# Kernel tuning notes

Hardware: AMD Instinct MI355X
Metric: run time of the kernel (lower is better)

## Reference

```python
import jax, jax.numpy as jnp
import numpy as np

B, C, T = 8, 1024, 1500          # batch, WavLM feature dim, frames
K = 8192                         # linguistic centroid bank size
D, H = 256, 512                  # refiner embed dim, MLP hidden dim
NQ, BINS = 4, 1024               # RVQ stages, codebook bins per stage
LRELU_SLOPE = 0.01               # torch LeakyReLU default
EPS = 1e-8


def setup_inputs():
    key = jax.random.key(0)
    ks = jax.random.split(key, 24)
    w = lambda k, s: jax.random.normal(k, s, dtype=jnp.float32) * 0.02
    inp = {
        'feature': jax.random.normal(ks[0], (B, C, T), dtype=jnp.float32),
        'centroid': jax.random.normal(ks[1], (K, C), dtype=jnp.float32),
        # SpeakerRefiner encoder: 1024->512->512->256 (LeakyReLU between)
        'enc_w0': w(ks[2], (C, H)), 'enc_b0': w(ks[3], (H,)),
        'enc_w1': w(ks[4], (H, H)), 'enc_b1': w(ks[5], (H,)),
        'enc_w2': w(ks[6], (H, D)), 'enc_b2': w(ks[7], (D,)),
        # SpeakerRefiner decoder: 256->512->512->1024 (LeakyReLU between)
        'dec_w0': w(ks[8], (D, H)), 'dec_b0': w(ks[9], (H,)),
        'dec_w1': w(ks[10], (H, H)), 'dec_b1': w(ks[11], (H,)),
        'dec_w2': w(ks[12], (H, C)), 'dec_b2': w(ks[13], (C,)),
        # SpeakerNormalizer: 1024->512->512->256, ReLU after EVERY layer
        'nrm_w0': w(ks[14], (C, H)), 'nrm_b0': w(ks[15], (H,)),
        'nrm_w1': w(ks[16], (H, H)), 'nrm_b1': w(ks[17], (H,)),
        'nrm_w2': w(ks[18], (H, D)), 'nrm_b2': w(ks[19], (D,)),
        # RVQ codebooks, one per stage
        'codebooks': jax.random.normal(ks[20], (NQ, BINS, D), dtype=jnp.float32),
    }
    return inp


def _nn_gather(x_flat, table):
    """argmin of squared distances (x^2 - 2 x.C^T + C^2) + row gather."""
    dist = ((x_flat ** 2).sum(1, keepdims=True)
            - 2.0 * x_flat @ table.T
            + (table ** 2).sum(1)[None, :])
    idx = jnp.argmin(dist, axis=1)
    return table[idx]


def reference(feature, centroid,
              enc_w0, enc_b0, enc_w1, enc_b1, enc_w2, enc_b2,
              dec_w0, dec_b0, dec_w1, dec_b1, dec_w2, dec_b2,
              nrm_w0, nrm_b0, nrm_w1, nrm_b1, nrm_w2, nrm_b2,
              codebooks):
    lrelu = lambda v: jax.nn.leaky_relu(v, LRELU_SLOPE)

    def enc(z):  # (B,T,C) -> (B,T,D)
        h0 = lrelu(z @ enc_w0 + enc_b0)
        h1 = lrelu(h0 @ enc_w1 + enc_b1)
        return h1 @ enc_w2 + enc_b2

    def dec(z):  # (B,T,D) -> (B,T,C)
        h0 = lrelu(z @ dec_w0 + dec_b0)
        h1 = lrelu(h0 @ dec_w1 + dec_b1)
        return h1 @ dec_w2 + dec_b2

    def nrm(z):  # (B,T,C) -> (B,T,D), ReLU after each Linear
        h0 = jax.nn.relu(z @ nrm_w0 + nrm_b0)
        h1 = jax.nn.relu(h0 @ nrm_w1 + nrm_b1)
        return jax.nn.relu(h1 @ nrm_w2 + nrm_b2)

    # ---- linguistic VQ: cdist + argmin + gather over centroid bank ----
    x_flat = feature.transpose(0, 2, 1).reshape(-1, C)        # (B*T, C)
    lin_dec_bt = _nn_gather(x_flat, centroid).reshape(B, T, C)  # (B,T,C)
    lin_dec = lin_dec_bt.transpose(0, 2, 1)                    # (B,C,T)

    # ---- speaker residual path ----
    spk_raw = feature - lin_dec                                # (B,C,T)
    spk_enc = enc(spk_raw.transpose(0, 2, 1))                  # (B,T,D)
    norm_vec = nrm(lin_dec_bt)                                 # (B,T,D)  (iteration > norm_start_step branch)
    spk_enc_norm = spk_enc / (norm_vec + EPS)

    # ---- residual vector quantizer (n_q stages, straight-through) ----
    residual, q_sum = spk_enc_norm, jnp.zeros_like(spk_enc_norm)
    for i in range(NQ):
        q = _nn_gather(residual.reshape(-1, D), codebooks[i]).reshape(B, T, D)
        q_sum = q_sum + q
        residual = residual - q
    quantized = spk_enc_norm + jax.lax.stop_gradient(q_sum - spk_enc_norm)

    # ---- denorm + decode + combine ----
    spk_enc_denorm = quantized * norm_vec
    spk_dec = dec(spk_enc_denorm).transpose(0, 2, 1)           # (B,C,T)
    dec_feature = lin_dec + spk_dec                            # quantize == [1,1]
    return dec_feature
```

## Files before the change

### kernel.cpp

```cpp
#include <hip/hip_runtime.h>

namespace {

constexpr int kB = 8;
constexpr int kC = 1024;
constexpr int kT = 1500;
constexpr int kK = 8192;
constexpr int kD = 256;
constexpr int kH = 512;
constexpr int kNQ = 4;
constexpr int kBins = 1024;
constexpr int kN = kB * kT;
constexpr float kEps = 1e-8f;
constexpr float kSlope = 0.01f;
constexpr float kMargin = 8.0f;
constexpr unsigned kCap = 4194304;

using u64 = unsigned long long;
typedef __attribute__((ext_vector_type(8))) short bf16x8;
typedef __attribute__((ext_vector_type(4))) float f32x4;

__device__ __forceinline__ unsigned ordered_bits(float f) {
  unsigned b = __float_as_uint(f);
  return (b & 0x80000000u) ? ~b : (b | 0x80000000u);
}
__device__ __forceinline__ float unordered_bits(unsigned b) {
  return __uint_as_float((b & 0x80000000u) ? (b ^ 0x80000000u) : ~b);
}
__device__ __forceinline__ unsigned short f2bf(float f) {
  unsigned u = __float_as_uint(f);
  return (unsigned short)((u + 0x7fffu + ((u >> 16) & 1u)) >> 16);
}
__device__ __forceinline__ void gl_lds16(const void* g, void* l) {
  __builtin_amdgcn_global_load_lds(
      (const __attribute__((address_space(1))) void*)g,
      (__attribute__((address_space(3))) void*)l, 16, 0, 0);
}

__global__ __launch_bounds__(256) void transpose_in(const float* __restrict__ f,
                                                    float* __restrict__ X) {
  __shared__ float tile[32][33];
  const int t0 = blockIdx.x * 32, c0 = blockIdx.y * 32, b = blockIdx.z;
  const int tx = threadIdx.x, ty = threadIdx.y;
#pragma unroll
  for (int i = 0; i < 4; ++i) {
    const int cl = ty + i * 8;
    if (t0 + tx < kT)
      tile[cl][tx] = f[(size_t)b * kC * kT + (size_t)(c0 + cl) * kT + (t0 + tx)];
  }
  __syncthreads();
#pragma unroll
  for (int i = 0; i < 4; ++i) {
    const int tl = ty + i * 8;
    if (t0 + tl < kT)
      X[(size_t)(b * kT + t0 + tl) * kC + (c0 + tx)] = tile[tx][tl];
  }
}

__global__ __launch_bounds__(256) void to_bf16(const float* __restrict__ in,
                                               unsigned short* __restrict__ out,
                                               int n4) {
  const int i = blockIdx.x * 256 + threadIdx.x;
  if (i >= n4) return;
  const float4 v = reinterpret_cast<const float4*>(in)[i];
  ushort4 o;
  o.x = f2bf(v.x); o.y = f2bf(v.y); o.z = f2bf(v.z); o.w = f2bf(v.w);
  reinterpret_cast<ushort4*>(out)[i] = o;
}

__global__ __launch_bounds__(256) void row_sqsum(const float* __restrict__ A,
                                                 float* __restrict__ S, int Kd) {
  const int r = blockIdx.x;
  const float4* a4 = reinterpret_cast<const float4*>(A + (size_t)r * Kd);
  float s = 0.f;
  for (int i = threadIdx.x; i < (Kd >> 2); i += 256) {
    const float4 v = a4[i];
    s = fmaf(v.x, v.x, s); s = fmaf(v.y, v.y, s);
    s = fmaf(v.z, v.z, s); s = fmaf(v.w, v.w, s);
  }
#pragma unroll
  for (int off = 32; off > 0; off >>= 1) s += __shfl_down(s, off, 64);
  __shared__ float ws[4];
  const int lane = threadIdx.x & 63, w = threadIdx.x >> 6;
  if (lane == 0) ws[w] = s;
  __syncthreads();
  if (threadIdx.x == 0) S[r] = (ws[0] + ws[1]) + (ws[2] + ws[3]);
}

__global__ __launch_bounds__(256) void lin_vq_mfma(
    const unsigned short* __restrict__ Ah, const unsigned short* __restrict__ Bh,
    const float* __restrict__ S, const float* __restrict__ cc,
    unsigned* __restrict__ rowmin, unsigned* __restrict__ cands,
    unsigned* __restrict__ counter, int M) {
  __shared__ __attribute__((aligned(16))) unsigned short lsa[128 * 32];
  __shared__ __attribute__((aligned(16))) unsigned short lsb[128 * 32];
  const int t = threadIdx.x;
  const int l = t & 63, w = t >> 6;
  const int wr = w >> 1, wc = w & 1;
  const int m0 = blockIdx.x * 128, n0 = blockIdx.y * 128;
  const int rl = l & 15, lh = l >> 4;
  const int srow = l >> 2, sp = l & 3;
  f32x4 acc[4][4] = {};
  for (int k0 = 0; k0 < kC; k0 += 32) {
#pragma unroll
    for (int i = 0; i < 2; ++i) {
      const int rb = (w * 2 + i) * 16;
      const int r = rb + srow;
      const int s = (sp - ((r >> 1) & 3)) & 3;
      gl_lds16(Ah + ((size_t)(m0 + r) * kC + k0 + s * 8), &lsa[rb * 32]);
      gl_lds16(Bh + ((size_t)(n0 + r) * kC + k0 + s * 8), &lsb[rb * 32]);
    }
    __syncthreads();
    bf16x8 a[4], b[4];
#pragma unroll
    for (int m = 0; m < 4; ++m) {
      const int r = wr * 64 + m * 16 + rl;
      const int pp = (lh + ((r >> 1) & 3)) & 3;
      a[m] = *reinterpret_cast<const bf16x8*>(&lsa[r * 32 + pp * 8]);
    }
#pragma unroll
    for (int n = 0; n < 4; ++n) {
      const int r = wc * 64 + n * 16 + rl;
      const int pp = (lh + ((r >> 1) & 3)) & 3;
      b[n] = *reinterpret_cast<const bf16x8*>(&lsb[r * 32 + pp * 8]);
    }
#pragma unroll
    for (int m = 0; m < 4; ++m)
#pragma unroll
      for (int n = 0; n < 4; ++n)
        acc[m][n] = __builtin_amdgcn_mfma_f32_16x16x32_bf16(a[m], b[n], acc[m][n], 0, 0, 0);
    __syncthreads();
  }
  float ccv[4];
#pragma unroll
  for (int n = 0; n < 4; ++n) ccv[n] = cc[n0 + wc * 64 + n * 16 + rl];
#pragma unroll
  for (int m = 0; m < 4; ++m) {
#pragma unroll
    for (int j = 0; j < 4; ++j) {
      const int gr = m0 + wr * 64 + m * 16 + lh * 4 + j;
      const bool valid = gr < M;
      const float Sv = valid ? S[gr] : 0.f;
      float mn = 3.4e38f;
#pragma unroll
      for (int n = 0; n < 4; ++n) {
        const float d = fmaf(-2.f, acc[m][n][j], Sv) + ccv[n];
        acc[m][n][j] = d;
        mn = fminf(mn, d);
      }
#pragma unroll
      for (int mask = 1; mask < 16; mask <<= 1)
        mn = fminf(mn, __shfl_xor(mn, mask, 64));
      if (valid && rl == 0) atomicMin(&rowmin[gr], ordered_bits(mn));
    }
  }
  __threadfence();
#pragma unroll
  for (int m = 0; m < 4; ++m) {
#pragma unroll
    for (int j = 0; j < 4; ++j) {
      const int gr = m0 + wr * 64 + m * 16 + lh * 4 + j;
      if (gr >= M) continue;
      const float thr = unordered_bits(rowmin[gr]) + kMargin;
#pragma unroll
      for (int n = 0; n < 4; ++n) {
        if (acc[m][n][j] <= thr) {
          const unsigned gc = (unsigned)(n0 + wc * 64 + n * 16 + rl);
          const unsigned slot = atomicAdd(counter, 1u);
          if (slot < kCap) cands[slot] = (unsigned)gr * 8192u + gc;
        }
      }
    }
  }
}

__global__ __launch_bounds__(256) void rescore(
    const float* __restrict__ X, const float* __restrict__ Cn,
    const float* __restrict__ S, const float* __restrict__ cc,
    const unsigned* __restrict__ cands, const unsigned* __restrict__ counter,
    u64* __restrict__ keys) {
  const unsigned nc = min(*counter, kCap);
  const int l = threadIdx.x & 63;
  const unsigned wglob = (blockIdx.x * 256 + threadIdx.x) >> 6;
  const unsigned nw = (gridDim.x * 256) >> 6;
  for (unsigned i = wglob; i < nc; i += nw) {
    const unsigned pc = cands[i];
    const int r = pc >> 13, c = pc & 8191;
    const float4* xr = reinterpret_cast<const float4*>(X + (size_t)r * kC);
    const float4* cr = reinterpret_cast<const float4*>(Cn + (size_t)c * kC);
    float acc = 0.f;
#pragma unroll
    for (int q = 0; q < 4; ++q) {
      const float4 a = xr[l * 4 + q], b = cr[l * 4 + q];
      acc = fmaf(a.x, b.x, acc); acc = fmaf(a.y, b.y, acc);
      acc = fmaf(a.z, b.z, acc); acc = fmaf(a.w, b.w, acc);
    }
#pragma unroll
    for (int off = 32; off > 0; off >>= 1) acc += __shfl_down(acc, off, 64);
    if (l == 0) {
      const float d = (S[r] - 2.0f * acc) + cc[c];
      atomicMin(&keys[r], ((u64)ordered_bits(d) << 32) | (unsigned)c);
    }
  }
}

__global__ __launch_bounds__(256) void vq_argmin(
    const float* __restrict__ A, const float* __restrict__ table,
    const float* __restrict__ cc, const float* __restrict__ S,
    u64* __restrict__ keys, int M, int Kd) {
  __shared__ float As[16][128];
  __shared__ float Ts[16][128];
  __shared__ u64 red[128][16];
  const int m0 = blockIdx.x * 128, n0 = blockIdx.y * 128;
  const int t = threadIdx.x;
  const int tx = t & 15, ty = t >> 4;
  const int lrow = t >> 1, lk8 = (t & 1) * 8;
  float acc[8][8] = {};
  for (int k0 = 0; k0 < Kd; k0 += 16) {
    const int gm = m0 + lrow;
    float4 a0 = make_float4(0.f, 0.f, 0.f, 0.f), a1 = a0;
    if (gm < M) {
      const float* ap = &A[(size_t)gm * Kd + (k0 + lk8)];
      a0 = *reinterpret_cast<const float4*>(ap);
      a1 = *reinterpret_cast<const float4*>(ap + 4);
    }
    const float* tp = &table[(size_t)(n0 + lrow) * Kd + (k0 + lk8)];
    const float4 b0 = *reinterpret_cast<const float4*>(tp);
    const float4 b1 = *reinterpret_cast<const float4*>(tp + 4);
    As[lk8 + 0][lrow] = a0.x; As[lk8 + 1][lrow] = a0.y;
    As[lk8 + 2][lrow] = a0.z; As[lk8 + 3][lrow] = a0.w;
    As[lk8 + 4][lrow] = a1.x; As[lk8 + 5][lrow] = a1.y;
    As[lk8 + 6][lrow] = a1.z; As[lk8 + 7][lrow] = a1.w;
    Ts[lk8 + 0][lrow] = b0.x; Ts[lk8 + 1][lrow] = b0.y;
    Ts[lk8 + 2][lrow] = b0.z; Ts[lk8 + 3][lrow] = b0.w;
    Ts[lk8 + 4][lrow] = b1.x; Ts[lk8 + 5][lrow] = b1.y;
    Ts[lk8 + 6][lrow] = b1.z; Ts[lk8 + 7][lrow] = b1.w;
    __syncthreads();
#pragma unroll
    for (int kk = 0; kk < 16; ++kk) {
      float ar[8], br[8];
      *reinterpret_cast<float4*>(&ar[0]) = *reinterpret_cast<const float4*>(&As[kk][ty * 8]);
      *reinterpret_cast<float4*>(&ar[4]) = *reinterpret_cast<const float4*>(&As[kk][ty * 8 + 4]);
      *reinterpret_cast<float4*>(&br[0]) = *reinterpret_cast<const float4*>(&Ts[kk][tx * 8]);
      *reinterpret_cast<float4*>(&br[4]) = *reinterpret_cast<const float4*>(&Ts[kk][tx * 8 + 4]);
#pragma unroll
      for (int i = 0; i < 8; ++i)
#pragma unroll
        for (int j = 0; j < 8; ++j) acc[i][j] = fmaf(ar[i], br[j], acc[i][j]);
    }
    __syncthreads();
  }
  float ccv[8];
  *reinterpret_cast<float4*>(&ccv[0]) = *reinterpret_cast<const float4*>(&cc[n0 + tx * 8]);
  *reinterpret_cast<float4*>(&ccv[4]) = *reinterpret_cast<const float4*>(&cc[n0 + tx * 8 + 4]);
#pragma unroll
  for (int i = 0; i < 8; ++i) {
    const int gm = m0 + ty * 8 + i;
    const float Srow = (gm < M) ? S[gm] : 0.f;
    u64 best = ~0ull;
#pragma unroll
    for (int j = 0; j < 8; ++j) {
      const int gn = n0 + tx * 8 + j;
      const float d = (Srow - 2.0f * acc[i][j]) + ccv[j];
      const u64 key = ((u64)ordered_bits(d) << 32) | (unsigned)gn;
      best = (key < best) ? key : best;
    }
    red[ty * 8 + i][tx] = best;
  }
  __syncthreads();
  if (t < 128) {
    u64 b = red[t][0];
#pragma unroll
    for (int j = 1; j < 16; ++j) { const u64 v = red[t][j]; b = (v < b) ? v : b; }
    const int gm = m0 + t;
    if (gm < M) atomicMin(&keys[gm], b);
  }
}

__global__ __launch_bounds__(256) void gather_residual(
    const float* __restrict__ centroid, const u64* __restrict__ keys,
    float* __restrict__ X, float* __restrict__ lin_dec) {
  const int i4 = blockIdx.x * 256 + threadIdx.x;
  const int n = i4 >> 8;
  const int c4 = (i4 & 255) << 2;
  const unsigned idx = (unsigned)(keys[n] & 0xffffffffu);
  const float4 cv = *reinterpret_cast<const float4*>(&centroid[(size_t)idx * kC + c4]);
  float4 xv = *reinterpret_cast<const float4*>(&X[(size_t)n * kC + c4]);
  xv.x -= cv.x; xv.y -= cv.y; xv.z -= cv.z; xv.w -= cv.w;
  *reinterpret_cast<float4*>(&lin_dec[(size_t)n * kC + c4]) = cv;
  *reinterpret_cast<float4*>(&X[(size_t)n * kC + c4]) = xv;
}

template <int ACT>
__global__ __launch_bounds__(256) void gemm_bias_act(
    const float* __restrict__ A, const float* __restrict__ W,
    const float* __restrict__ bias, float* __restrict__ out,
    int M, int Nc, int Kd) {
  __shared__ float As[16][64];
  __shared__ float Ws[16][64];
  const int m0 = blockIdx.x * 64, n0 = blockIdx.y * 64;
  const int t = threadIdx.x;
  const int tx = t & 15, ty = t >> 4;
  const int arow = t >> 2, ak4 = (t & 3) << 2;
  const int wk = t >> 4, wn4 = (t & 15) << 2;
  float acc[4][4] = {};
  for (int k0 = 0; k0 < Kd; k0 += 16) {
    float4 av = make_float4(0.f, 0.f, 0.f, 0.f);
    const int gm = m0 + arow;
    if (gm < M) av = *reinterpret_cast<const float4*>(&A[(size_t)gm * Kd + (k0 + ak4)]);
    As[ak4 + 0][arow] = av.x; As[ak4 + 1][arow] = av.y;
    As[ak4 + 2][arow] = av.z; As[ak4 + 3][arow] = av.w;
    *reinterpret_cast<float4*>(&Ws[wk][wn4]) =
        *reinterpret_cast<const float4*>(&W[(size_t)(k0 + wk) * Nc + (n0 + wn4)]);
    __syncthreads();
#pragma unroll
    for (int kk = 0; kk < 16; ++kk) {
      float ar[4], br[4];
      *reinterpret_cast<float4*>(ar) = *reinterpret_cast<const float4*>(&As[kk][ty << 2]);
      *reinterpret_cast<float4*>(br) = *reinterpret_cast<const float4*>(&Ws[kk][tx << 2]);
#pragma unroll
      for (int i = 0; i < 4; ++i)
#pragma unroll
        for (int j = 0; j < 4; ++j) acc[i][j] = fmaf(ar[i], br[j], acc[i][j]);
    }
    __syncthreads();
  }
  float bv[4];
  *reinterpret_cast<float4*>(bv) = *reinterpret_cast<const float4*>(&bias[n0 + (tx << 2)]);
#pragma unroll
  for (int i = 0; i < 4; ++i) {
    const int gm = m0 + (ty << 2) + i;
    if (gm >= M) continue;
    float o[4];
#pragma unroll
    for (int j = 0; j < 4; ++j) {
      float v = acc[i][j] + bv[j];
      if (ACT == 1) v = (v >= 0.f) ? v : kSlope * v;
      if (ACT == 2) v = fmaxf(v, 0.f);
      o[j] = v;
    }
    *reinterpret_cast<float4*>(&out[(size_t)gm * Nc + n0 + (tx << 2)]) =
        *reinterpret_cast<const float4*>(o);
  }
}

__global__ __launch_bounds__(256) void norm_div_init(
    const float* __restrict__ e, const float* __restrict__ nv,
    float* __restrict__ resid, float* __restrict__ qsum) {
  const int i = blockIdx.x * 256 + threadIdx.x;
  const float4 ev = reinterpret_cast<const float4*>(e)[i];
  const float4 vv = reinterpret_cast<const float4*>(nv)[i];
  float4 r;
  r.x = ev.x / (vv.x + kEps); r.y = ev.y / (vv.y + kEps);
  r.z = ev.z / (vv.z + kEps); r.w = ev.w / (vv.w + kEps);
  reinterpret_cast<float4*>(resid)[i] = r;
  reinterpret_cast<float4*>(qsum)[i] = make_float4(0.f, 0.f, 0.f, 0.f);
}

__global__ __launch_bounds__(256) void rvq_update(
    const float* __restrict__ cb, const u64* __restrict__ keys,
    float* __restrict__ resid, float* __restrict__ qsum) {
  const int i4 = blockIdx.x * 256 + threadIdx.x;
  const int n = i4 >> 6;
  const int d4 = (i4 & 63) << 2;
  const unsigned idx = (unsigned)(keys[n] & 0xffffffffu);
  const float4 q = *reinterpret_cast<const float4*>(&cb[(size_t)idx * kD + d4]);
  float4 r = reinterpret_cast<float4*>(resid)[i4];
  float4 s = reinterpret_cast<float4*>(qsum)[i4];
  r.x -= q.x; r.y -= q.y; r.z -= q.z; r.w -= q.w;
  s.x += q.x; s.y += q.y; s.z += q.z; s.w += q.w;
  reinterpret_cast<float4*>(resid)[i4] = r;
  reinterpret_cast<float4*>(qsum)[i4] = s;
}

__global__ __launch_bounds__(256) void denorm(
    const float* __restrict__ qsum, const float* __restrict__ nv,
    float* __restrict__ o) {
  const int i = blockIdx.x * 256 + threadIdx.x;
  const float4 q = reinterpret_cast<const float4*>(qsum)[i];
  const float4 v = reinterpret_cast<const float4*>(nv)[i];
  float4 r;
  r.x = q.x * v.x; r.y = q.y * v.y; r.z = q.z * v.z; r.w = q.w * v.w;
  reinterpret_cast<float4*>(o)[i] = r;
}

__global__ __launch_bounds__(256) void final_out(const float* __restrict__ lin_dec,
                                                 const float* __restrict__ dec_out,
                                                 float* __restrict__ out) {
  __shared__ float tile[32][33];
  const int t0 = blockIdx.x * 32, c0 = blockIdx.y * 32, b = blockIdx.z;
  const int tx = threadIdx.x, ty = threadIdx.y;
#pragma unroll
  for (int i = 0; i < 4; ++i) {
    const int tl = ty + i * 8;
    if (t0 + tl < kT) {
      const size_t idx = (size_t)(b * kT + t0 + tl) * kC + (c0 + tx);
      tile[tl][tx] = lin_dec[idx] + dec_out[idx];
    }
  }
  __syncthreads();
#pragma unroll
  for (int i = 0; i < 4; ++i) {
    const int cl = ty + i * 8;
    if (t0 + tx < kT)
      out[(size_t)b * kC * kT + (size_t)(c0 + cl) * kT + (t0 + tx)] = tile[tx][cl];
  }
}

}

extern "C" void kernel_launch(void* const* d_in, const int* in_sizes, int n_in,
                              void* d_out, int out_size, void* d_ws, size_t ws_size,
                              hipStream_t stream) {
  (void)in_sizes; (void)n_in; (void)out_size; (void)ws_size;
  const float* feature  = (const float*)d_in[0];
  const float* centroid = (const float*)d_in[1];
  const float* enc_w0 = (const float*)d_in[2];  const float* enc_b0 = (const float*)d_in[3];
  const float* enc_w1 = (const float*)d_in[4];  const float* enc_b1 = (const float*)d_in[5];
  const float* enc_w2 = (const float*)d_in[6];  const float* enc_b2 = (const float*)d_in[7];
  const float* dec_w0 = (const float*)d_in[8];  const float* dec_b0 = (const float*)d_in[9];
  const float* dec_w1 = (const float*)d_in[10]; const float* dec_b1 = (const float*)d_in[11];
  const float* dec_w2 = (const float*)d_in[12]; const float* dec_b2 = (const float*)d_in[13];
  const float* nrm_w0 = (const float*)d_in[14]; const float* nrm_b0 = (const float*)d_in[15];
  const float* nrm_w1 = (const float*)d_in[16]; const float* nrm_b1 = (const float*)d_in[17];
  const float* nrm_w2 = (const float*)d_in[18]; const float* nrm_b2 = (const float*)d_in[19];
  const float* codebooks = (const float*)d_in[20];
  float* out = (float*)d_out;

  float* X       = (float*)d_ws;
  float* lin_dec = X       + (size_t)kN * kC;
  float* h0      = lin_dec + (size_t)kN * kC;
  float* h1      = h0      + (size_t)kN * kH;
  float* e_out   = h1      + (size_t)kN * kH;
  float* nvec    = e_out   + (size_t)kN * kD;
  float* resid   = nvec    + (size_t)kN * kD;
  float* qsum    = resid   + (size_t)kN * kD;
  float* Srow    = qsum    + (size_t)kN * kD;
  float* ccbuf   = Srow    + kN;
  u64*   keys    = (u64*)(ccbuf + kK);

  unsigned short* xh = (unsigned short*)h0;
  unsigned short* ch = (unsigned short*)h1;
  unsigned* cands    = (unsigned*)lin_dec;
  unsigned* rowmin   = (unsigned*)(h1 + 4500000);
  unsigned* counter  = rowmin + kN;

  const dim3 tb32(32, 8);
  const dim3 tgT((kT + 31) / 32, kC / 32, kB);

  transpose_in<<<tgT, tb32, 0, stream>>>(feature, X);

  row_sqsum<<<kN, 256, 0, stream>>>(X, Srow, kC);
  row_sqsum<<<kK, 256, 0, stream>>>(centroid, ccbuf, kC);
  to_bf16<<<(kN * kC / 4 + 255) / 256, 256, 0, stream>>>(X, xh, kN * kC / 4);
  to_bf16<<<(kK * kC / 4 + 255) / 256, 256, 0, stream>>>(centroid, ch, kK * kC / 4);
  hipMemsetAsync(rowmin, 0xFF, (size_t)kN * sizeof(unsigned), stream);
  hipMemsetAsync(counter, 0x00, sizeof(unsigned), stream);
  hipMemsetAsync(keys, 0xFF, (size_t)kN * sizeof(u64), stream);
  lin_vq_mfma<<<dim3((kN + 127) / 128, kK / 128), 256, 0, stream>>>(
      xh, ch, Srow, ccbuf, rowmin, cands, counter, kN);
  rescore<<<512, 256, 0, stream>>>(X, centroid, Srow, ccbuf, cands, counter, keys);
  gather_residual<<<kN * kC / 4 / 256, 256, 0, stream>>>(centroid, keys, X, lin_dec);

  const dim3 gH((kN + 63) / 64, kH / 64);
  const dim3 gD((kN + 63) / 64, kD / 64);
  const dim3 gC((kN + 63) / 64, kC / 64);

  gemm_bias_act<1><<<gH, 256, 0, stream>>>(X,  enc_w0, enc_b0, h0,    kN, kH, kC);
  gemm_bias_act<1><<<gH, 256, 0, stream>>>(h0, enc_w1, enc_b1, h1,    kN, kH, kH);
  gemm_bias_act<0><<<gD, 256, 0, stream>>>(h1, enc_w2, enc_b2, e_out, kN, kD, kH);

  gemm_bias_act<2><<<gH, 256, 0, stream>>>(lin_dec, nrm_w0, nrm_b0, h0,   kN, kH, kC);
  gemm_bias_act<2><<<gH, 256, 0, stream>>>(h0,      nrm_w1, nrm_b1, h1,   kN, kH, kH);
  gemm_bias_act<2><<<gD, 256, 0, stream>>>(h1,      nrm_w2, nrm_b2, nvec, kN, kD, kH);

  norm_div_init<<<kN * kD / 4 / 256, 256, 0, stream>>>(e_out, nvec, resid, qsum);

  for (int q = 0; q < kNQ; ++q) {
    const float* cb = codebooks + (size_t)q * kBins * kD;
    row_sqsum<<<kN, 256, 0, stream>>>(resid, Srow, kD);
    row_sqsum<<<kBins, 256, 0, stream>>>(cb, ccbuf, kD);
    hipMemsetAsync(keys, 0xFF, (size_t)kN * sizeof(u64), stream);
    vq_argmin<<<dim3((kN + 127) / 128, kBins / 128), 256, 0, stream>>>(
        resid, cb, ccbuf, Srow, keys, kN, kD);
    rvq_update<<<kN * kD / 4 / 256, 256, 0, stream>>>(cb, keys, resid, qsum);
  }

  denorm<<<kN * kD / 4 / 256, 256, 0, stream>>>(qsum, nvec, e_out);

  gemm_bias_act<1><<<gH, 256, 0, stream>>>(e_out, dec_w0, dec_b0, h0, kN, kH, kD);
  gemm_bias_act<1><<<gH, 256, 0, stream>>>(h0,    dec_w1, dec_b1, h1, kN, kH, kH);
  gemm_bias_act<0><<<gC, 256, 0, stream>>>(h1,    dec_w2, dec_b2, X,  kN, kC, kH);

  final_out<<<tgT, tb32, 0, stream>>>(lin_dec, X, out);
}
```

Measured before the change: 2.794 ms.

## Move decoder MLP to bf16 MFMA GEMMs and double-buffer the centroid search GEMM

The three decoder GEMMs move from the fp32 gemm_bias_act kernel to a new bf16 MFMA kernel. It uses double-buffered LDS staging and writes bf16 intermediate activations. The decoder weights are transposed to bf16 on device, and the denorm step now writes bf16 directly. The lin_vq_mfma kernel gets double-buffered async global-to-LDS loads and a block-index swizzle that groups blocks for cache locality. The change trades decoder precision (bf16 inputs and hidden states) for matrix-core throughput, and adds a few small transpose launches.

```diff
diff --git a/kernel.cpp b/kernel.cpp
--- a/kernel.cpp
+++ b/kernel.cpp
@@ -37,6 +37,19 @@
       (__attribute__((address_space(3))) void*)l, 16, 0, 0);
 }
 
+__device__ __forceinline__ void stage_tile(const unsigned short* __restrict__ g,
+                                           int rowlen, int r0, int k0,
+                                           unsigned short* lds,
+                                           int w, int srow, int sp) {
+#pragma unroll
+  for (int i = 0; i < 2; ++i) {
+    const int rb = (w * 2 + i) * 16;
+    const int r = rb + srow;
+    const int s = (sp - ((r >> 1) & 3)) & 3;
+    gl_lds16(g + ((size_t)(r0 + r) * rowlen + k0 + s * 8), lds + rb * 32);
+  }
+}
+
 __global__ __launch_bounds__(256) void transpose_in(const float* __restrict__ f,
                                                     float* __restrict__ X) {
   __shared__ float tile[32][33];
@@ -68,6 +81,20 @@
   reinterpret_cast<ushort4*>(out)[i] = o;
 }
 
+__global__ __launch_bounds__(256) void transpose_w_bf16(
+    const float* __restrict__ W, unsigned short* __restrict__ WT, int K, int N) {
+  __shared__ float tile[32][33];
+  const int k0 = blockIdx.x * 32, n0 = blockIdx.y * 32;
+  const int tx = threadIdx.x, ty = threadIdx.y;
+#pragma unroll
+  for (int i = 0; i < 4; ++i)
+    tile[ty + i * 8][tx] = W[(size_t)(k0 + ty + i * 8) * N + (n0 + tx)];
+  __syncthreads();
+#pragma unroll
+  for (int i = 0; i < 4; ++i)
+    WT[(size_t)(n0 + ty + i * 8) * K + (k0 + tx)] = f2bf(tile[tx][ty + i * 8]);
+}
+
 __global__ __launch_bounds__(256) void row_sqsum(const float* __restrict__ A,
                                                  float* __restrict__ S, int Kd) {
   const int r = blockIdx.x;
@@ -92,37 +119,41 @@
     const float* __restrict__ S, const float* __restrict__ cc,
     unsigned* __restrict__ rowmin, unsigned* __restrict__ cands,
     unsigned* __restrict__ counter, int M) {
-  __shared__ __attribute__((aligned(16))) unsigned short lsa[128 * 32];
-  __shared__ __attribute__((aligned(16))) unsigned short lsb[128 * 32];
+  __shared__ __attribute__((aligned(16))) unsigned short lsa[2][128 * 32];
+  __shared__ __attribute__((aligned(16))) unsigned short lsb[2][128 * 32];
   const int t = threadIdx.x;
   const int l = t & 63, w = t >> 6;
   const int wr = w >> 1, wc = w & 1;
-  const int m0 = blockIdx.x * 128, n0 = blockIdx.y * 128;
   const int rl = l & 15, lh = l >> 4;
   const int srow = l >> 2, sp = l & 3;
+  const unsigned nbx = gridDim.x;
+  const unsigned flat = blockIdx.y * nbx + blockIdx.x;
+  const unsigned q8 = (nbx * gridDim.y) >> 3;
+  const unsigned swz = (flat & 7u) * q8 + (flat >> 3);
+  const int m0 = (int)(swz % nbx) * 128, n0 = (int)(swz / nbx) * 128;
+
   f32x4 acc[4][4] = {};
-  for (int k0 = 0; k0 < kC; k0 += 32) {
-#pragma unroll
-    for (int i = 0; i < 2; ++i) {
-      const int rb = (w * 2 + i) * 16;
-      const int r = rb + srow;
-      const int s = (sp - ((r >> 1) & 3)) & 3;
-      gl_lds16(Ah + ((size_t)(m0 + r) * kC + k0 + s * 8), &lsa[rb * 32]);
-      gl_lds16(Bh + ((size_t)(n0 + r) * kC + k0 + s * 8), &lsb[rb * 32]);
-    }
-    __syncthreads();
+  stage_tile(Ah, kC, m0, 0, lsa[0], w, srow, sp);
+  stage_tile(Bh, kC, n0, 0, lsb[0], w, srow, sp);
+  __syncthreads();
+  for (int kt = 0; kt < kC / 32; ++kt) {
+    const int p = kt & 1;
+    if (kt + 1 < kC / 32) {
+      stage_tile(Ah, kC, m0, (kt + 1) * 32, lsa[p ^ 1], w, srow, sp);
+      stage_tile(Bh, kC, n0, (kt + 1) * 32, lsb[p ^ 1], w, srow, sp);
+    }
     bf16x8 a[4], b[4];
 #pragma unroll
     for (int m = 0; m < 4; ++m) {
       const int r = wr * 64 + m * 16 + rl;
       const int pp = (lh + ((r >> 1) & 3)) & 3;
-      a[m] = *reinterpret_cast<const bf16x8*>(&lsa[r * 32 + pp * 8]);
+      a[m] = *reinterpret_cast<const bf16x8*>(&lsa[p][r * 32 + pp * 8]);
     }
 #pragma unroll
     for (int n = 0; n < 4; ++n) {
       const int r = wc * 64 + n * 16 + rl;
       const int pp = (lh + ((r >> 1) & 3)) & 3;
-      b[n] = *reinterpret_cast<const bf16x8*>(&lsb[r * 32 + pp * 8]);
+      b[n] = *reinterpret_cast<const bf16x8*>(&lsb[p][r * 32 + pp * 8]);
     }
 #pragma unroll
     for (int m = 0; m < 4; ++m)
@@ -169,6 +200,77 @@
           const unsigned slot = atomicAdd(counter, 1u);
           if (slot < kCap) cands[slot] = (unsigned)gr * 8192u + gc;
         }
+      }
+    }
+  }
+}
+
+template <int ACT, int OUTBF>
+__global__ __launch_bounds__(256) void gemm_bf16(
+    const unsigned short* __restrict__ A, const unsigned short* __restrict__ WT,
+    const float* __restrict__ bias, void* __restrict__ outp,
+    int M, int N, int K) {
+  __shared__ __attribute__((aligned(16))) unsigned short lsa[2][128 * 32];
+  __shared__ __attribute__((aligned(16))) unsigned short lsb[2][128 * 32];
+  const int t = threadIdx.x;
+  const int l = t & 63, w = t >> 6;
+  const int wr = w >> 1, wc = w & 1;
+  const int rl = l & 15, lh = l >> 4;
+  const int srow = l >> 2, sp = l & 3;
+  const unsigned nbx = gridDim.x;
+  const unsigned nwg = nbx * gridDim.y;
+  const unsigned flat = blockIdx.y * nbx + blockIdx.x;
+  unsigned swz = flat;
+  if ((nwg & 7u) == 0) swz = (flat & 7u) * (nwg >> 3) + (flat >> 3);
+  const int m0 = (int)(swz % nbx) * 128, n0 = (int)(swz / nbx) * 128;
+
+  f32x4 acc[4][4] = {};
+  stage_tile(A, K, m0, 0, lsa[0], w, srow, sp);
+  stage_tile(WT, K, n0, 0, lsb[0], w, srow, sp);
+  __syncthreads();
+  const int NT = K >> 5;
+  for (int kt = 0; kt < NT; ++kt) {
+    const int p = kt & 1;
+    if (kt + 1 < NT) {
+      stage_tile(A, K, m0, (kt + 1) * 32, lsa[p ^ 1], w, srow, sp);
+      stage_tile(WT, K, n0, (kt + 1) * 32, lsb[p ^ 1], w, srow, sp);
+    }
+    bf16x8 a[4], b[4];
+#pragma unroll
+    for (int m = 0; m < 4; ++m) {
+      const int r = wr * 64 + m * 16 + rl;
+      const int pp = (lh + ((r >> 1) & 3)) & 3;
+      a[m] = *reinterpret_cast<const bf16x8*>(&lsa[p][r * 32 + pp * 8]);
+    }
+#pragma unroll
+    for (int n = 0; n < 4; ++n) {
+      const int r = wc * 64 + n * 16 + rl;
+      const int pp = (lh + ((r >> 1) & 3)) & 3;
+      b[n] = *reinterpret_cast<const bf16x8*>(&lsb[p][r * 32 + pp * 8]);
+    }
+#pragma unroll
+    for (int m = 0; m < 4; ++m)
+#pragma unroll
+      for (int n = 0; n < 4; ++n)
+        acc[m][n] = __builtin_amdgcn_mfma_f32_16x16x32_bf16(a[m], b[n], acc[m][n], 0, 0, 0);
+    __syncthreads();
+  }
+  float bv[4];
+#pragma unroll
+  for (int n = 0; n < 4; ++n) bv[n] = bias[n0 + wc * 64 + n * 16 + rl];
+#pragma unroll
+  for (int m = 0; m < 4; ++m) {
+#pragma unroll
+    for (int j = 0; j < 4; ++j) {
+      const int gr = m0 + wr * 64 + m * 16 + lh * 4 + j;
+      if (gr >= M) continue;
+#pragma unroll
+      for (int n = 0; n < 4; ++n) {
+        float v = acc[m][n][j] + bv[n];
+        if (ACT == 1) v = (v >= 0.f) ? v : kSlope * v;
+        const int gc = n0 + wc * 64 + n * 16 + rl;
+        if (OUTBF) ((unsigned short*)outp)[(size_t)gr * N + gc] = f2bf(v);
+        else       ((float*)outp)[(size_t)gr * N + gc] = v;
       }
     }
   }
@@ -373,15 +475,16 @@
   reinterpret_cast<float4*>(qsum)[i4] = s;
 }
 
-__global__ __launch_bounds__(256) void denorm(
+__global__ __launch_bounds__(256) void denorm_bf16(
     const float* __restrict__ qsum, const float* __restrict__ nv,
-    float* __restrict__ o) {
+    unsigned short* __restrict__ o) {
   const int i = blockIdx.x * 256 + threadIdx.x;
   const float4 q = reinterpret_cast<const float4*>(qsum)[i];
   const float4 v = reinterpret_cast<const float4*>(nv)[i];
-  float4 r;
-  r.x = q.x * v.x; r.y = q.y * v.y; r.z = q.z * v.z; r.w = q.w * v.w;
-  reinterpret_cast<float4*>(o)[i] = r;
+  ushort4 r;
+  r.x = f2bf(q.x * v.x); r.y = f2bf(q.y * v.y);
+  r.z = f2bf(q.z * v.z); r.w = f2bf(q.w * v.w);
+  reinterpret_cast<ushort4*>(o)[i] = r;
 }
 
 __global__ __launch_bounds__(256) void final_out(const float* __restrict__ lin_dec,
@@ -444,6 +547,12 @@
   unsigned* cands    = (unsigned*)lin_dec;
   unsigned* rowmin   = (unsigned*)(h1 + 4500000);
   unsigned* counter  = rowmin + kN;
+  unsigned short* dec_in_bf = (unsigned short*)e_out;
+  unsigned short* h0b = (unsigned short*)h0;
+  unsigned short* h1b = (unsigned short*)h1;
+  unsigned short* wT0 = (unsigned short*)(h0 + 3200000);
+  unsigned short* wT1 = wT0 + (size_t)kH * kD;
+  unsigned short* wT2 = wT1 + (size_t)kH * kH;
 
   const dim3 tb32(32, 8);
   const dim3 tgT((kT + 31) / 32, kC / 32, kB);
@@ -464,7 +573,6 @@
 
   const dim3 gH((kN + 63) / 64, kH / 64);
   const dim3 gD((kN + 63) / 64, kD / 64);
-  const dim3 gC((kN + 63) / 64, kC / 64);
 
   gemm_bias_act<1><<<gH, 256, 0, stream>>>(X,  enc_w0, enc_b0, h0,    kN, kH, kC);
   gemm_bias_act<1><<<gH, 256, 0, stream>>>(h0, enc_w1, enc_b1, h1,    kN, kH, kH);
@@ -486,11 +594,16 @@
     rvq_update<<<kN * kD / 4 / 256, 256, 0, stream>>>(cb, keys, resid, qsum);
   }
 
-  denorm<<<kN * kD / 4 / 256, 256, 0, stream>>>(qsum, nvec, e_out);
-
-  gemm_bias_act<1><<<gH, 256, 0, stream>>>(e_out, dec_w0, dec_b0, h0, kN, kH, kD);
-  gemm_bias_act<1><<<gH, 256, 0, stream>>>(h0,    dec_w1, dec_b1, h1, kN, kH, kH);
-  gemm_bias_act<0><<<gC, 256, 0, stream>>>(h1,    dec_w2, dec_b2, X,  kN, kC, kH);
+  transpose_w_bf16<<<dim3(kD / 32, kH / 32), tb32, 0, stream>>>(dec_w0, wT0, kD, kH);
+  transpose_w_bf16<<<dim3(kH / 32, kH / 32), tb32, 0, stream>>>(dec_w1, wT1, kH, kH);
+  transpose_w_bf16<<<dim3(kH / 32, kC / 32), tb32, 0, stream>>>(dec_w2, wT2, kH, kC);
+  denorm_bf16<<<kN * kD / 4 / 256, 256, 0, stream>>>(qsum, nvec, dec_in_bf);
+  gemm_bf16<1, 1><<<dim3((kN + 127) / 128, kH / 128), 256, 0, stream>>>(
+      dec_in_bf, wT0, dec_b0, h0b, kN, kH, kD);
+  gemm_bf16<1, 1><<<dim3((kN + 127) / 128, kH / 128), 256, 0, stream>>>(
+      h0b, wT1, dec_b1, h1b, kN, kH, kH);
+  gemm_bf16<0, 0><<<dim3((kN + 127) / 128, kC / 128), 256, 0, stream>>>(
+      h1b, wT2, dec_b2, X, kN, kC, kH);
 
   final_out<<<tgT, tb32, 0, stream>>>(lin_dec, X, out);
 }
```

Result: faster. 2.469 ms (-11.6%).
